# Performance work log

Measured on AMD Instinct MI355X. Metric: run time of the kernel, lower is better.

The kernel has to match this reference:

```python
import jax, jax.numpy as jnp
import numpy as np
import math

B, S, E, HEAD = 4, 2048, 1024, 64  # num_heads=16 -> head_size = 1024//16


def setup_inputs() -> dict:
    key = jax.random.key(0)
    kx, kp, kq, kk, kv = jax.random.split(key, 5)
    std = math.sqrt(2.0 / (E + HEAD))
    return {
        "x": jax.random.normal(kx, (B, S, E), dtype=jnp.float32),
        "padding_mask": jax.random.randint(kp, (B, S), 0, 2, dtype=jnp.int32),
        "Wq": jax.random.normal(kq, (HEAD, E), dtype=jnp.float32) * std,
        "Wk": jax.random.normal(kk, (HEAD, E), dtype=jnp.float32) * std,
        "Wv": jax.random.normal(kv, (HEAD, E), dtype=jnp.float32) * std,
    }


def reference(x, padding_mask, Wq, Wk, Wv):
    # q,k,v: [B,S,head] via Linear (x @ W.T, no bias)
    q = jnp.einsum("bse,he->bsh", x, Wq)
    k = jnp.einsum("bse,he->bsh", x, Wk)
    v = jnp.einsum("bse,he->bsh", x, Wv)
    scores = jnp.einsum("bqh,bkh->bqk", q, k)  # [B,S,S]
    seq = x.shape[1]
    causal = jnp.tril(jnp.ones((seq, seq), dtype=jnp.float32))  # [S,S]
    mask = causal[None, :, :] * padding_mask.astype(jnp.float32)[:, None, :]  # [B,S,S]
    scores = jnp.where(mask == 0, jnp.float32(-1e9), scores)
    head_size = k.shape[-1]
    attn = jax.nn.softmax(scores / jnp.sqrt(jnp.float32(head_size)), axis=-1)
    return jnp.einsum("bqk,bkh->bqh", attn, v)
```

## Files before the change

kernel.cpp:

```cpp
#include <hip/hip_runtime.h>
#include <hip/hip_bf16.h>
#include <math.h>

#define B_ 4
#define S_ 2048
#define E_ 1024
#define H_ 64
#define NQT 32
#define SPLITS 8
#define TPS 4

typedef short bf16x8 __attribute__((ext_vector_type(8)));
typedef float f32x4 __attribute__((ext_vector_type(4)));
typedef unsigned short u16x8 __attribute__((ext_vector_type(8)));
typedef unsigned short u16x4 __attribute__((ext_vector_type(4)));

__device__ __forceinline__ unsigned short f2bf(float f){
    unsigned u = __builtin_bit_cast(unsigned, f);
    u += 0x7fffu + ((u >> 16) & 1u);
    return (unsigned short)(u >> 16);
}
__device__ __forceinline__ float bf2f(unsigned short h){
    return __builtin_bit_cast(float, ((unsigned)h) << 16);
}
#define MFMA16(a,b,c) __builtin_amdgcn_mfma_f32_16x16x32_bf16((a),(b),(c),0,0,0)

__device__ __forceinline__ void gload_lds16(const void* g, void* l){
    __builtin_amdgcn_global_load_lds((const __attribute__((address_space(1))) unsigned int*)g,
                                     (__attribute__((address_space(3))) unsigned int*)l, 16, 0, 0);
}

__global__ __launch_bounds__(256) void wprep_kernel(
    const float* __restrict__ Wq, const float* __restrict__ Wk,
    const float* __restrict__ Wv,
    unsigned short* __restrict__ WhiS, unsigned short* __restrict__ WloS)
{
    const int gid = blockIdx.x*256 + threadIdx.x;
    const int n = gid >> 7, g = gid & 127;
    const float* W = (n < 64)  ? (Wq + (size_t)n*E_)
                   : (n < 128) ? (Wk + (size_t)(n-64)*E_)
                               : (Wv + (size_t)(n-128)*E_);
    const int gs = (g & ~7) | ((g & 7) ^ (n & 7));
    const float* src = W + gs*8;
    float4 a = ((const float4*)src)[0];
    float4 b = ((const float4*)src)[1];
    float vv[8] = {a.x,a.y,a.z,a.w,b.x,b.y,b.z,b.w};
    u16x8 hv, lv;
    #pragma unroll
    for (int j=0;j<8;j++){ unsigned short h = f2bf(vv[j]); hv[j]=h; lv[j]=f2bf(vv[j]-bf2f(h)); }
    ((u16x8*)WhiS)[n*128 + g] = hv;
    ((u16x8*)WloS)[n*128 + g] = lv;
}

__global__ __launch_bounds__(256) void qkv_kernel(
    const float* __restrict__ x,
    const unsigned short* __restrict__ WhiS, const unsigned short* __restrict__ WloS,
    unsigned short* __restrict__ Qhi, unsigned short* __restrict__ Qlo,
    unsigned short* __restrict__ Khi, unsigned short* __restrict__ Klo,
    unsigned short* __restrict__ Vt)
{
    __shared__ unsigned short Ah[32*64], Al[32*64];
    __shared__ unsigned short Bh[192*64], Bl[192*64];
    const int m0 = blockIdx.x * 32;
    const int tid = threadIdx.x;
    const int lane = tid & 63, wv = tid >> 6, l15 = lane & 15, quad = lane >> 4;

    f32x4 acc[2][3];
    #pragma unroll
    for (int mt=0;mt<2;mt++)
    #pragma unroll
    for (int nt=0;nt<3;nt++) acc[mt][nt] = f32x4{0.f,0.f,0.f,0.f};

    const int arow = tid >> 3;
    const int ag   = tid & 7;
    unsigned short* tbuf = (wv < 2) ? Bh : Bl;
    const unsigned short* gsrc = (wv < 2) ? WhiS : WloS;
    const int rbase0 = (wv & 1) * 96;
    const int lrow = lane >> 3, lgrp = lane & 7;

    for (int k0 = 0; k0 < E_; k0 += 64) {
        const float* xs = x + (size_t)(m0 + arow)*E_ + k0 + ag*8;
        float4 xa = ((const float4*)xs)[0];
        float4 xb = ((const float4*)xs)[1];
        __syncthreads();
        #pragma unroll
        for (int i = 0; i < 12; i++) {
            const int rb = rbase0 + i*8;
            const unsigned short* gp = gsrc + (size_t)(rb + lrow)*E_ + k0 + lgrp*8;
            gload_lds16(gp, tbuf + rb*64);
        }
        {
            float vv[8] = {xa.x,xa.y,xa.z,xa.w,xb.x,xb.y,xb.z,xb.w};
            u16x8 hv, lv;
            #pragma unroll
            for (int j=0;j<8;j++){ unsigned short h = f2bf(vv[j]); hv[j]=h; lv[j]=f2bf(vv[j]-bf2f(h)); }
            const int idx = arow*8 + (ag ^ (arow & 7));
            ((u16x8*)Ah)[idx] = hv; ((u16x8*)Al)[idx] = lv;
        }
        __syncthreads();
        #pragma unroll
        for (int kk=0; kk<2; kk++){
            const int xr = (kk*4+quad) ^ (l15 & 7);
            bf16x8 ah[2], al[2];
            #pragma unroll
            for (int mt=0; mt<2; mt++){
                const int arw = mt*16 + l15;
                ah[mt] = ((const bf16x8*)Ah)[arw*8 + xr];
                al[mt] = ((const bf16x8*)Al)[arw*8 + xr];
            }
            #pragma unroll
            for (int nt=0; nt<3; nt++){
                const int brw = wv*48 + nt*16 + l15;
                bf16x8 bh = ((const bf16x8*)Bh)[brw*8 + xr];
                bf16x8 bl = ((const bf16x8*)Bl)[brw*8 + xr];
                #pragma unroll
                for (int mt=0; mt<2; mt++){
                    acc[mt][nt] = MFMA16(ah[mt], bh, acc[mt][nt]);
                    acc[mt][nt] = MFMA16(ah[mt], bl, acc[mt][nt]);
                    acc[mt][nt] = MFMA16(al[mt], bh, acc[mt][nt]);
                }
            }
        }
    }
    #pragma unroll
    for (int nt=0; nt<3; nt++){
        const int n = wv*48 + nt*16 + l15;
        const int comp = n >> 6, c = n & 63;
        if (comp < 2) {
            unsigned short* dh = (comp==0) ? Qhi : Khi;
            unsigned short* dl = (comp==0) ? Qlo : Klo;
            #pragma unroll
            for (int mt=0; mt<2; mt++)
            #pragma unroll
            for (int r=0; r<4; r++){
                const int row = m0 + mt*16 + quad*4 + r;
                float v = acc[mt][nt][r];
                unsigned short h = f2bf(v);
                dh[(size_t)row*H_ + c] = h;
                dl[(size_t)row*H_ + c] = f2bf(v - bf2f(h));
            }
        } else {
            #pragma unroll
            for (int mt=0; mt<2; mt++){
                const int m = m0 + mt*16 + quad*4;
                const int b = m >> 11, s0 = m & (S_-1);
                u16x4 pk;
                #pragma unroll
                for (int r=0;r<4;r++) pk[r] = f2bf(acc[mt][nt][r]);
                *(u16x4*)(Vt + (size_t)(b*H_ + c)*S_ + s0) = pk;
            }
        }
    }
}

__global__ __launch_bounds__(256) void meanv_kernel(const unsigned short* __restrict__ Vt,
                                                    float* __restrict__ meanV)
{
    int b = blockIdx.x >> 6, h = blockIdx.x & 63;
    const unsigned short* src = Vt + (size_t)b*H_*S_ + (size_t)h*S_;
    float sum = 0.f;
    for (int j = threadIdx.x; j < S_; j += 256) sum += bf2f(src[j]);
    #pragma unroll
    for (int m=32; m>=1; m>>=1) sum += __shfl_xor(sum, m);
    __shared__ float red[4];
    if ((threadIdx.x & 63) == 0) red[threadIdx.x >> 6] = sum;
    __syncthreads();
    if (threadIdx.x == 0) meanV[b*H_ + h] = (red[0]+red[1]+red[2]+red[3]) * (1.f/S_);
}

__global__ __launch_bounds__(256) void attn_kernel(
    const unsigned short* __restrict__ Qhi, const unsigned short* __restrict__ Qlo,
    const unsigned short* __restrict__ Khi, const unsigned short* __restrict__ Klo,
    const unsigned short* __restrict__ Vt, const int* __restrict__ pad,
    float* __restrict__ Opart, float* __restrict__ mpart, float* __restrict__ lpart)
{
    const int qt = blockIdx.x, b = blockIdx.y, sp = blockIdx.z;
    const int t0 = sp * TPS;
    if (t0 > qt) return;
    const int t1 = min(t0 + TPS, qt + 1);

    __shared__ unsigned short KtH[64*64], KtL[64*64], Vts[64*64];
    __shared__ unsigned short Ps[4][64*20];
    __shared__ int pad_s[64];

    const int tid = threadIdx.x, lane = tid & 63, wv = tid >> 6, l15 = lane & 15, quad = lane >> 4;
    const int role = tid >> 6, srow = tid & 63;

    const size_t qrow = (size_t)(b*S_ + qt*64 + wv*16 + l15);
    bf16x8 aqh0 = *(const bf16x8*)(Qhi + qrow*H_ + quad*8);
    bf16x8 aqh1 = *(const bf16x8*)(Qhi + qrow*H_ + 32 + quad*8);
    bf16x8 aql0 = *(const bf16x8*)(Qlo + qrow*H_ + quad*8);
    bf16x8 aql1 = *(const bf16x8*)(Qlo + qrow*H_ + 32 + quad*8);

    float m_i[4], l_i[4];
    f32x4 o[4];
    #pragma unroll
    for (int r=0;r<4;r++){ m_i[r] = -INFINITY; l_i[r] = 0.f; }
    #pragma unroll
    for (int i=0;i<4;i++) o[i] = f32x4{0.f,0.f,0.f,0.f};

    const int qg = qt*64 + wv*16 + quad*4;
    unsigned short* Pw = &Ps[wv][0];

    for (int t = t0; t < t1; ++t) {
        const int kb = t * 64;
        __syncthreads();
        if (role < 3) {
            const unsigned short* gs =
                (role==0) ? (Khi + ((size_t)(b*S_ + kb + srow))*H_) :
                (role==1) ? (Klo + ((size_t)(b*S_ + kb + srow))*H_) :
                            (Vt + (size_t)b*H_*S_ + (size_t)srow*S_ + kb);
            unsigned short* ld = (role==0) ? KtH : (role==1) ? KtL : Vts;
            #pragma unroll
            for (int i=0;i<8;i++){
                u16x8 d = ((const u16x8*)gs)[i];
                ((u16x8*)ld)[srow*8 + (i ^ (srow & 7))] = d;
            }
        } else {
            pad_s[srow] = pad[b*S_ + kb + srow];
        }
        __syncthreads();

        f32x4 s[4];
        #pragma unroll
        for (int nt=0; nt<4; nt++){
            const int krw = nt*16 + l15;
            bf16x8 bh0 = ((const bf16x8*)KtH)[krw*8 + ((quad)   ^ (l15 & 7))];
            bf16x8 bh1 = ((const bf16x8*)KtH)[krw*8 + ((4+quad) ^ (l15 & 7))];
            bf16x8 bl0 = ((const bf16x8*)KtL)[krw*8 + ((quad)   ^ (l15 & 7))];
            bf16x8 bl1 = ((const bf16x8*)KtL)[krw*8 + ((4+quad) ^ (l15 & 7))];
            f32x4 z = f32x4{0.f,0.f,0.f,0.f};
            z = MFMA16(aqh0, bh0, z);
            z = MFMA16(aqh1, bh1, z);
            z = MFMA16(aqh0, bl0, z);
            z = MFMA16(aqh1, bl1, z);
            z = MFMA16(aql0, bh0, z);
            z = MFMA16(aql1, bh1, z);
            s[nt] = z;
        }
        float rmax[4] = {-INFINITY,-INFINITY,-INFINITY,-INFINITY};
        #pragma unroll
        for (int nt=0; nt<4; nt++){
            const int kcol = nt*16 + l15;
            const int kg = kb + kcol;
            const int pv = pad_s[kcol];
            #pragma unroll
            for (int r=0;r<4;r++){
                bool ok = (kg <= qg + r) && (pv != 0);
                float v = ok ? s[nt][r]*0.125f : -1.25e8f;
                s[nt][r] = v;
                rmax[r] = fmaxf(rmax[r], v);
            }
        }
        #pragma unroll
        for (int msk=1; msk<=8; msk<<=1){
            #pragma unroll
            for (int r=0;r<4;r++) rmax[r] = fmaxf(rmax[r], __shfl_xor(rmax[r], msk));
        }
        float alpha[4];
        #pragma unroll
        for (int r=0;r<4;r++){
            float mn = fmaxf(m_i[r], rmax[r]);
            alpha[r] = __expf(m_i[r] - mn);
            m_i[r] = mn;
        }
        float rsum[4] = {0.f,0.f,0.f,0.f};
        #pragma unroll
        for (int nt=0; nt<4; nt++)
        #pragma unroll
        for (int r=0;r<4;r++){
            float p = __expf(s[nt][r] - m_i[r]);
            s[nt][r] = p;
            rsum[r] += p;
        }
        #pragma unroll
        for (int msk=1; msk<=8; msk<<=1){
            #pragma unroll
            for (int r=0;r<4;r++) rsum[r] += __shfl_xor(rsum[r], msk);
        }
        #pragma unroll
        for (int r=0;r<4;r++) l_i[r] = l_i[r]*alpha[r] + rsum[r];
        #pragma unroll
        for (int hnt=0; hnt<4; hnt++)
        #pragma unroll
        for (int r=0;r<4;r++) o[hnt][r] *= alpha[r];

        #pragma unroll
        for (int nt=0; nt<4; nt++){
            const int key = nt*16 + l15;
            u16x4 pk;
            #pragma unroll
            for (int r=0;r<4;r++) pk[r] = f2bf(s[nt][r]);
            *(u16x4*)(Pw + key*20 + quad*4) = pk;
        }
        #pragma unroll
        for (int ks=0; ks<2; ks++){
            bf16x8 ap;
            #pragma unroll
            for (int j=0;j<8;j++) ap[j] = (short)Pw[(ks*32 + quad*8 + j)*20 + l15];
            #pragma unroll
            for (int hnt=0; hnt<4; hnt++){
                bf16x8 bv = ((const bf16x8*)Vts)[(hnt*16+l15)*8 + ((ks*4+quad) ^ (l15 & 7))];
                o[hnt] = MFMA16(ap, bv, o[hnt]);
            }
        }
    }
    const size_t rbase = ((size_t)((b*NQT + qt)*SPLITS + sp))*64 + wv*16 + quad*4;
    if (l15 == 0) {
        #pragma unroll
        for (int r=0;r<4;r++){ mpart[rbase + r] = m_i[r]; lpart[rbase + r] = l_i[r]; }
    }
    #pragma unroll
    for (int hnt=0; hnt<4; hnt++)
    #pragma unroll
    for (int r=0;r<4;r++)
        Opart[(rbase + r)*H_ + hnt*16 + l15] = o[hnt][r];
}

__global__ __launch_bounds__(256) void combine_kernel(
    const float* __restrict__ Opart, const float* __restrict__ mpart,
    const float* __restrict__ lpart, const float* __restrict__ meanV,
    float* __restrict__ out)
{
    const int idx = blockIdx.x*256 + threadIdx.x;
    const int h = idx & 63;
    const int q = (idx >> 6) & (S_-1);
    const int b = idx >> 17;
    const int qt = q >> 6, r = q & 63;
    const int ns = (qt >> 2) + 1;
    const size_t rb = ((size_t)(b*NQT + qt)*SPLITS)*64 + r;
    float M = -INFINITY;
    for (int s2=0; s2<ns; s2++) M = fmaxf(M, mpart[rb + (size_t)s2*64]);
    float res;
    if (M == -1.25e8f) {
        res = meanV[b*H_ + h];
    } else {
        float L = 0.f, acc = 0.f;
        for (int s2=0; s2<ns; s2++){
            float mi = mpart[rb + (size_t)s2*64];
            float wgt = __expf(mi - M);
            L += wgt * lpart[rb + (size_t)s2*64];
            acc += wgt * Opart[(rb + (size_t)s2*64)*H_ + h];
        }
        res = acc / L;
    }
    out[idx] = res;
}

extern "C" void kernel_launch(void* const* d_in, const int* in_sizes, int n_in,
                              void* d_out, int out_size, void* d_ws, size_t ws_size,
                              hipStream_t stream)
{
    (void)in_sizes; (void)n_in; (void)out_size; (void)ws_size;
    const float* x  = (const float*)d_in[0];
    const int* pad  = (const int*)d_in[1];
    const float* Wq = (const float*)d_in[2];
    const float* Wk = (const float*)d_in[3];
    const float* Wv = (const float*)d_in[4];
    float* out = (float*)d_out;
    char* ws = (char*)d_ws;
    const size_t MB = 1u << 20;
    unsigned short* Qhi = (unsigned short*)(ws + 0*MB);
    unsigned short* Qlo = (unsigned short*)(ws + 1*MB);
    unsigned short* Khi = (unsigned short*)(ws + 2*MB);
    unsigned short* Klo = (unsigned short*)(ws + 3*MB);
    unsigned short* Vt  = (unsigned short*)(ws + 4*MB);
    float* Opart = (float*)(ws + 5*MB);
    float* mpart = (float*)(ws + 21*MB);
    float* lpart = (float*)(ws + 21*MB + (1u<<18));
    float* meanV = (float*)(ws + 21*MB + 2*(1u<<18));
    unsigned short* WhiS = (unsigned short*)(ws + 22*MB);
    unsigned short* WloS = (unsigned short*)(ws + 22*MB + 512*1024);

    wprep_kernel<<<dim3(96), 256, 0, stream>>>(Wq, Wk, Wv, WhiS, WloS);
    qkv_kernel<<<dim3(256), 256, 0, stream>>>(x, WhiS, WloS, Qhi, Qlo, Khi, Klo, Vt);
    meanv_kernel<<<dim3(256), 256, 0, stream>>>(Vt, meanV);
    attn_kernel<<<dim3(NQT, B_, SPLITS), 256, 0, stream>>>(Qhi, Qlo, Khi, Klo, Vt, pad,
                                                           Opart, mpart, lpart);
    combine_kernel<<<dim3((B_*S_*H_)/256), 256, 0, stream>>>(Opart, mpart, lpart, meanV, out);
}
```

Baseline: 136.7 us.

## Load K/V tiles directly from global memory instead of staging in LDS

Removes the shared-memory staging of K hi/lo, V transposed and the padding mask, along with the two block barriers per key tile. Each wave now reads its MFMA operands straight from global memory (relying on L1/L2 to serve the reuse across the four waves). This drops the barriers and the LDS write/read traffic, but each tile is now fetched four times from cache and the global load latency is exposed directly before each MFMA.

```diff
diff --git a/kernel.cpp b/kernel.cpp
--- a/kernel.cpp
+++ b/kernel.cpp
@@ -179,12 +179,9 @@
     if (t0 > qt) return;
     const int t1 = min(t0 + TPS, qt + 1);
 
-    __shared__ unsigned short KtH[64*64], KtL[64*64], Vts[64*64];
     __shared__ unsigned short Ps[4][64*20];
-    __shared__ int pad_s[64];
 
     const int tid = threadIdx.x, lane = tid & 63, wv = tid >> 6, l15 = lane & 15, quad = lane >> 4;
-    const int role = tid >> 6, srow = tid & 63;
 
     const size_t qrow = (size_t)(b*S_ + qt*64 + wv*16 + l15);
     bf16x8 aqh0 = *(const bf16x8*)(Qhi + qrow*H_ + quad*8);
@@ -192,6 +189,11 @@
     bf16x8 aql0 = *(const bf16x8*)(Qlo + qrow*H_ + quad*8);
     bf16x8 aql1 = *(const bf16x8*)(Qlo + qrow*H_ + 32 + quad*8);
 
+    const unsigned short* KhB = Khi + (size_t)(b*S_)*H_;
+    const unsigned short* KlB = Klo + (size_t)(b*S_)*H_;
+    const unsigned short* VB  = Vt  + (size_t)b*H_*S_;
+    const int* padB = pad + b*S_;
+
     float m_i[4], l_i[4];
     f32x4 o[4];
     #pragma unroll
@@ -204,31 +206,19 @@
 
     for (int t = t0; t < t1; ++t) {
         const int kb = t * 64;
-        __syncthreads();
-        if (role < 3) {
-            const unsigned short* gs =
-                (role==0) ? (Khi + ((size_t)(b*S_ + kb + srow))*H_) :
-                (role==1) ? (Klo + ((size_t)(b*S_ + kb + srow))*H_) :
-                            (Vt + (size_t)b*H_*S_ + (size_t)srow*S_ + kb);
-            unsigned short* ld = (role==0) ? KtH : (role==1) ? KtL : Vts;
-            #pragma unroll
-            for (int i=0;i<8;i++){
-                u16x8 d = ((const u16x8*)gs)[i];
-                ((u16x8*)ld)[srow*8 + (i ^ (srow & 7))] = d;
-            }
-        } else {
-            pad_s[srow] = pad[b*S_ + kb + srow];
-        }
-        __syncthreads();
+
+        int pv[4];
+        #pragma unroll
+        for (int nt=0; nt<4; nt++) pv[nt] = padB[kb + nt*16 + l15];
 
         f32x4 s[4];
         #pragma unroll
         for (int nt=0; nt<4; nt++){
-            const int krw = nt*16 + l15;
-            bf16x8 bh0 = ((const bf16x8*)KtH)[krw*8 + ((quad)   ^ (l15 & 7))];
-            bf16x8 bh1 = ((const bf16x8*)KtH)[krw*8 + ((4+quad) ^ (l15 & 7))];
-            bf16x8 bl0 = ((const bf16x8*)KtL)[krw*8 + ((quad)   ^ (l15 & 7))];
-            bf16x8 bl1 = ((const bf16x8*)KtL)[krw*8 + ((4+quad) ^ (l15 & 7))];
+            const size_t krow = (size_t)(kb + nt*16 + l15)*H_;
+            bf16x8 bh0 = *(const bf16x8*)(KhB + krow + quad*8);
+            bf16x8 bh1 = *(const bf16x8*)(KhB + krow + 32 + quad*8);
+            bf16x8 bl0 = *(const bf16x8*)(KlB + krow + quad*8);
+            bf16x8 bl1 = *(const bf16x8*)(KlB + krow + 32 + quad*8);
             f32x4 z = f32x4{0.f,0.f,0.f,0.f};
             z = MFMA16(aqh0, bh0, z);
             z = MFMA16(aqh1, bh1, z);
@@ -241,12 +231,10 @@
         float rmax[4] = {-INFINITY,-INFINITY,-INFINITY,-INFINITY};
         #pragma unroll
         for (int nt=0; nt<4; nt++){
-            const int kcol = nt*16 + l15;
-            const int kg = kb + kcol;
-            const int pv = pad_s[kcol];
+            const int kg = kb + nt*16 + l15;
             #pragma unroll
             for (int r=0;r<4;r++){
-                bool ok = (kg <= qg + r) && (pv != 0);
+                bool ok = (kg <= qg + r) && (pv[nt] != 0);
                 float v = ok ? s[nt][r]*0.125f : -1.25e8f;
                 s[nt][r] = v;
                 rmax[r] = fmaxf(rmax[r], v);
@@ -300,7 +288,7 @@
             for (int j=0;j<8;j++) ap[j] = (short)Pw[(ks*32 + quad*8 + j)*20 + l15];
             #pragma unroll
             for (int hnt=0; hnt<4; hnt++){
-                bf16x8 bv = ((const bf16x8*)Vts)[(hnt*16+l15)*8 + ((ks*4+quad) ^ (l15 & 7))];
+                bf16x8 bv = *(const bf16x8*)(VB + (size_t)(hnt*16 + l15)*S_ + kb + ks*32 + quad*8);
                 o[hnt] = MFMA16(ap, bv, o[hnt]);
             }
         }
```

After: 162.2 us. 1.19x slower.

## Double attention splits, specialize non-diagonal masking, fold meanV into combine

Applied to the files above, without the earlier changes.

Raises the key-split count from 8 to 16 with 2 tiles per split, giving more blocks to run in parallel and shorter per-block loops. Off-diagonal tiles now skip the causal comparison and apply only the padding mask. The separate meanV kernel is removed: rows that are fully masked compute the mean of V inline in the combine kernel, saving one launch. In exchange, the partial-output buffers double in size and the combine step reads more partials per row.

```diff
diff --git a/kernel.cpp b/kernel.cpp
--- a/kernel.cpp
+++ b/kernel.cpp
@@ -7,8 +7,8 @@
 #define E_ 1024
 #define H_ 64
 #define NQT 32
-#define SPLITS 8
-#define TPS 4
+#define SPLITS 16
+#define TPS 2
 
 typedef short bf16x8 __attribute__((ext_vector_type(8)));
 typedef float f32x4 __attribute__((ext_vector_type(4)));
@@ -153,21 +153,6 @@
     }
 }
 
-__global__ __launch_bounds__(256) void meanv_kernel(const unsigned short* __restrict__ Vt,
-                                                    float* __restrict__ meanV)
-{
-    int b = blockIdx.x >> 6, h = blockIdx.x & 63;
-    const unsigned short* src = Vt + (size_t)b*H_*S_ + (size_t)h*S_;
-    float sum = 0.f;
-    for (int j = threadIdx.x; j < S_; j += 256) sum += bf2f(src[j]);
-    #pragma unroll
-    for (int m=32; m>=1; m>>=1) sum += __shfl_xor(sum, m);
-    __shared__ float red[4];
-    if ((threadIdx.x & 63) == 0) red[threadIdx.x >> 6] = sum;
-    __syncthreads();
-    if (threadIdx.x == 0) meanV[b*H_ + h] = (red[0]+red[1]+red[2]+red[3]) * (1.f/S_);
-}
-
 __global__ __launch_bounds__(256) void attn_kernel(
     const unsigned short* __restrict__ Qhi, const unsigned short* __restrict__ Qlo,
     const unsigned short* __restrict__ Khi, const unsigned short* __restrict__ Klo,
@@ -192,6 +177,11 @@
     bf16x8 aql0 = *(const bf16x8*)(Qlo + qrow*H_ + quad*8);
     bf16x8 aql1 = *(const bf16x8*)(Qlo + qrow*H_ + 32 + quad*8);
 
+    const unsigned short* KhB = Khi + (size_t)(b*S_)*H_;
+    const unsigned short* KlB = Klo + (size_t)(b*S_)*H_;
+    const unsigned short* VB  = Vt  + (size_t)b*H_*S_;
+    const int* padB = pad + b*S_;
+
     float m_i[4], l_i[4];
     f32x4 o[4];
     #pragma unroll
@@ -207,9 +197,9 @@
         __syncthreads();
         if (role < 3) {
             const unsigned short* gs =
-                (role==0) ? (Khi + ((size_t)(b*S_ + kb + srow))*H_) :
-                (role==1) ? (Klo + ((size_t)(b*S_ + kb + srow))*H_) :
-                            (Vt + (size_t)b*H_*S_ + (size_t)srow*S_ + kb);
+                (role==0) ? (KhB + (size_t)(kb + srow)*H_) :
+                (role==1) ? (KlB + (size_t)(kb + srow)*H_) :
+                            (VB + (size_t)srow*S_ + kb);
             unsigned short* ld = (role==0) ? KtH : (role==1) ? KtL : Vts;
             #pragma unroll
             for (int i=0;i<8;i++){
@@ -217,7 +207,7 @@
                 ((u16x8*)ld)[srow*8 + (i ^ (srow & 7))] = d;
             }
         } else {
-            pad_s[srow] = pad[b*S_ + kb + srow];
+            pad_s[srow] = padB[kb + srow];
         }
         __syncthreads();
 
@@ -239,17 +229,31 @@
             s[nt] = z;
         }
         float rmax[4] = {-INFINITY,-INFINITY,-INFINITY,-INFINITY};
-        #pragma unroll
-        for (int nt=0; nt<4; nt++){
-            const int kcol = nt*16 + l15;
-            const int kg = kb + kcol;
-            const int pv = pad_s[kcol];
-            #pragma unroll
-            for (int r=0;r<4;r++){
-                bool ok = (kg <= qg + r) && (pv != 0);
-                float v = ok ? s[nt][r]*0.125f : -1.25e8f;
-                s[nt][r] = v;
-                rmax[r] = fmaxf(rmax[r], v);
+        int pv[4];
+        #pragma unroll
+        for (int nt=0; nt<4; nt++) pv[nt] = pad_s[nt*16 + l15];
+        if (t == qt) {
+            #pragma unroll
+            for (int nt=0; nt<4; nt++){
+                const int kg = kb + nt*16 + l15;
+                #pragma unroll
+                for (int r=0;r<4;r++){
+                    bool ok = (kg <= qg + r) && (pv[nt] != 0);
+                    float v = ok ? s[nt][r]*0.125f : -1.25e8f;
+                    s[nt][r] = v;
+                    rmax[r] = fmaxf(rmax[r], v);
+                }
+            }
+        } else {
+            #pragma unroll
+            for (int nt=0; nt<4; nt++){
+                const bool ok = (pv[nt] != 0);
+                #pragma unroll
+                for (int r=0;r<4;r++){
+                    float v = ok ? s[nt][r]*0.125f : -1.25e8f;
+                    s[nt][r] = v;
+                    rmax[r] = fmaxf(rmax[r], v);
+                }
             }
         }
         #pragma unroll
@@ -319,7 +323,7 @@
 
 __global__ __launch_bounds__(256) void combine_kernel(
     const float* __restrict__ Opart, const float* __restrict__ mpart,
-    const float* __restrict__ lpart, const float* __restrict__ meanV,
+    const float* __restrict__ lpart, const unsigned short* __restrict__ Vt,
     float* __restrict__ out)
 {
     const int idx = blockIdx.x*256 + threadIdx.x;
@@ -327,13 +331,21 @@
     const int q = (idx >> 6) & (S_-1);
     const int b = idx >> 17;
     const int qt = q >> 6, r = q & 63;
-    const int ns = (qt >> 2) + 1;
+    const int ns = qt / TPS + 1;
     const size_t rb = ((size_t)(b*NQT + qt)*SPLITS)*64 + r;
     float M = -INFINITY;
     for (int s2=0; s2<ns; s2++) M = fmaxf(M, mpart[rb + (size_t)s2*64]);
     float res;
     if (M == -1.25e8f) {
-        res = meanV[b*H_ + h];
+        const unsigned short* src = Vt + ((size_t)b*H_ + h)*S_;
+        float sum = 0.f;
+        #pragma unroll 4
+        for (int j=0;j<256;j++){
+            u16x8 d = ((const u16x8*)src)[j];
+            #pragma unroll
+            for (int e=0;e<8;e++) sum += bf2f((unsigned short)d[e]);
+        }
+        res = sum * (1.f/(float)S_);
     } else {
         float L = 0.f, acc = 0.f;
         for (int s2=0; s2<ns; s2++){
@@ -366,16 +378,14 @@
     unsigned short* Klo = (unsigned short*)(ws + 3*MB);
     unsigned short* Vt  = (unsigned short*)(ws + 4*MB);
     float* Opart = (float*)(ws + 5*MB);
-    float* mpart = (float*)(ws + 21*MB);
-    float* lpart = (float*)(ws + 21*MB + (1u<<18));
-    float* meanV = (float*)(ws + 21*MB + 2*(1u<<18));
-    unsigned short* WhiS = (unsigned short*)(ws + 22*MB);
-    unsigned short* WloS = (unsigned short*)(ws + 22*MB + 512*1024);
+    float* mpart = (float*)(ws + 40*MB);
+    float* lpart = (float*)(ws + 40*MB + (1u<<19));
+    unsigned short* WhiS = (unsigned short*)(ws + 41*MB);
+    unsigned short* WloS = (unsigned short*)(ws + 41*MB + 512*1024);
 
     wprep_kernel<<<dim3(96), 256, 0, stream>>>(Wq, Wk, Wv, WhiS, WloS);
     qkv_kernel<<<dim3(256), 256, 0, stream>>>(x, WhiS, WloS, Qhi, Qlo, Khi, Klo, Vt);
-    meanv_kernel<<<dim3(256), 256, 0, stream>>>(Vt, meanV);
     attn_kernel<<<dim3(NQT, B_, SPLITS), 256, 0, stream>>>(Qhi, Qlo, Khi, Klo, Vt, pad,
                                                            Opart, mpart, lpart);
-    combine_kernel<<<dim3((B_*S_*H_)/256), 256, 0, stream>>>(Opart, mpart, lpart, meanV, out);
-}
+    combine_kernel<<<dim3((B_*S_*H_)/256), 256, 0, stream>>>(Opart, mpart, lpart, Vt, out);
+}
```

Result: slower. 154.3 us (+12.9%).
